# Performance work log

Measured on AMD Instinct MI355X. Metric: run time of the kernel, lower is better.

Reference implementation:

```python
import jax, jax.numpy as jnp
import numpy as np

N_NODES = 50000
N_EDGES = 500000
D = 128
C = 50


def setup_inputs() -> dict:
    key = jax.random.key(0)
    k1, k2, k3, k4, k5, k6 = jax.random.split(key, 6)
    h = jax.random.normal(k1, (N_NODES, D), dtype=jnp.float32)
    e = jax.random.normal(k2, (N_EDGES, D), dtype=jnp.float32)
    src = jax.random.randint(k3, (N_EDGES,), 0, N_NODES, dtype=jnp.int64)
    dst = jax.random.randint(k4, (N_EDGES,), 0, N_NODES, dtype=jnp.int64)
    # nn.Linear(3*D, C): weight [C, 3*D], bias [C]
    W = jax.random.normal(k5, (C, 3 * D), dtype=jnp.float32) * (1.0 / np.sqrt(3 * D))
    b = jax.random.normal(k6, (C,), dtype=jnp.float32) * 0.01
    return {"h": h, "e": e, "src": src, "dst": dst, "W": W, "b": b}


def reference(h, e, src, dst, W, b):
    # gather node feats for each edge endpoint, concat with edge feats
    h_u = h[src]                                   # [E, D]
    h_v = h[dst]                                   # [E, D]
    feats = jnp.concatenate([h_u, h_v, e], axis=1)  # [E, 3D]
    score = jnp.einsum('ef,cf->ec', feats, W) + b   # [E, C]
    return score
```

## Files before the change

kernel.cpp:

```cpp
#include <hip/hip_runtime.h>
#include <hip/hip_bf16.h>

#define N_EDGES_C 500000
#define D_C 128
#define C_C 50
#define K3_C 384
#define CPAD_C 64

typedef __attribute__((ext_vector_type(8))) short bf16x8;
typedef __attribute__((ext_vector_type(4))) float f32x4;

static __device__ inline short2 pack_bf16_2(float a, float b) {
    union { __hip_bfloat162 h; short2 s; } u;
    u.h = __float22bfloat162_rn(make_float2(a, b));
    return u.s;
}

__global__ void wconv_kernel(const float* __restrict__ W, short* __restrict__ WB) {
    int idx = blockIdx.x * blockDim.x + threadIdx.x;
    if (idx >= CPAD_C * K3_C) return;
    int c = idx / K3_C;
    int k = idx - c * K3_C;
    float v = (c < C_C) ? W[c * K3_C + k] : 0.0f;
    union { __hip_bfloat16 b; short s; } u;
    u.b = __float2bfloat16(v);
    WB[idx] = u.s;
}

__global__ __launch_bounds__(256) void edge_mlp_kernel(
    const float* __restrict__ h, const float* __restrict__ ef,
    const int* __restrict__ src, const int* __restrict__ dst,
    const short* __restrict__ WB, const float* __restrict__ bias,
    float* __restrict__ out)
{
    const int lane = threadIdx.x & 63;
    const int wave = threadIdx.x >> 6;
    const int m = lane & 15;
    const int q = lane >> 4;
    const int kq = q * 8;

    const long wave_base = (long)blockIdx.x * 256 + (long)wave * 64;

    const float* psrc[4];
    const float* pdst[4];
    const float* pef[4];
#pragma unroll
    for (int i = 0; i < 4; ++i) {
        long ei = wave_base + i * 16 + m;
        long eic = ei < N_EDGES_C ? ei : (long)(N_EDGES_C - 1);
        int si = src[eic];
        int di = dst[eic];
        psrc[i] = h + (long)si * D_C + kq;
        pdst[i] = h + (long)di * D_C + kq;
        pef[i]  = ef + eic * D_C + kq;
    }

    const short* wrow[4];
#pragma unroll
    for (int t = 0; t < 4; ++t)
        wrow[t] = WB + (t * 16 + m) * K3_C + kq;

    f32x4 acc[4][4];
#pragma unroll
    for (int i = 0; i < 4; ++i)
#pragma unroll
        for (int t = 0; t < 4; ++t)
            acc[i][t] = (f32x4){0.0f, 0.0f, 0.0f, 0.0f};

    auto kstep = [&](const float* const (&pr)[4], int koff, int ko) {
        bf16x8 bfr[4];
#pragma unroll
        for (int t = 0; t < 4; ++t)
            bfr[t] = *reinterpret_cast<const bf16x8*>(wrow[t] + ko);
#pragma unroll
        for (int i = 0; i < 4; ++i) {
            const float4 f0 = *reinterpret_cast<const float4*>(pr[i] + koff);
            const float4 f1 = *reinterpret_cast<const float4*>(pr[i] + koff + 4);
            short2 p0 = pack_bf16_2(f0.x, f0.y);
            short2 p1 = pack_bf16_2(f0.z, f0.w);
            short2 p2 = pack_bf16_2(f1.x, f1.y);
            short2 p3 = pack_bf16_2(f1.z, f1.w);
            bf16x8 afr = { p0.x, p0.y, p1.x, p1.y, p2.x, p2.y, p3.x, p3.y };
#pragma unroll
            for (int t = 0; t < 4; ++t)
                acc[i][t] = __builtin_amdgcn_mfma_f32_16x16x32_bf16(afr, bfr[t], acc[i][t], 0, 0, 0);
        }
    };

#pragma unroll
    for (int kk = 0; kk < 128; kk += 32) kstep(psrc, kk, kk);
#pragma unroll
    for (int kk = 0; kk < 128; kk += 32) kstep(pdst, kk, 128 + kk);
#pragma unroll
    for (int kk = 0; kk < 128; kk += 32) kstep(pef, kk, 256 + kk);

    float bv[4];
#pragma unroll
    for (int t = 0; t < 4; ++t) {
        int c = t * 16 + m;
        bv[t] = (c < C_C) ? bias[c] : 0.0f;
    }
#pragma unroll
    for (int i = 0; i < 4; ++i) {
        long er0 = wave_base + i * 16 + q * 4;
#pragma unroll
        for (int r = 0; r < 4; ++r) {
            long ei = er0 + r;
            if (ei < N_EDGES_C) {
#pragma unroll
                for (int t = 0; t < 4; ++t) {
                    int c = t * 16 + m;
                    if (c < C_C) out[ei * (long)C_C + c] = acc[i][t][r] + bv[t];
                }
            }
        }
    }
}

extern "C" void kernel_launch(void* const* d_in, const int* in_sizes, int n_in,
                              void* d_out, int out_size, void* d_ws, size_t ws_size,
                              hipStream_t stream) {
    const float* h  = (const float*)d_in[0];
    const float* ef = (const float*)d_in[1];
    const int*   src = (const int*)d_in[2];
    const int*   dst = (const int*)d_in[3];
    const float* W  = (const float*)d_in[4];
    const float* b  = (const float*)d_in[5];
    float* out = (float*)d_out;
    short* WB  = (short*)d_ws;

    wconv_kernel<<<(CPAD_C * K3_C + 255) / 256, 256, 0, stream>>>(W, WB);

    const int nblocks = (N_EDGES_C + 255) / 256;
    edge_mlp_kernel<<<nblocks, 256, 0, stream>>>(h, ef, src, dst, WB, b, out);
}
```

Before: 481.2 us.

## Precompute per-node projections then gather them per edge instead of gathering raw features

Splits the linear layer by linearity: h is projected once per node through the src and dst slices of W, with the bias folded in, into a node table HW of 50000x128 floats. The edge kernel then runs a GEMM over only the edge-feature slice and adds two gathered 50-float rows from HW. This removes the gather of two 128-float node rows per edge and two thirds of the edge-side MFMA work. In exchange it adds a node GEMM pass and about 25MB of workspace traffic, and it falls back to the old path when the workspace is too small.

```diff
diff --git a/kernel.cpp b/kernel.cpp
--- a/kernel.cpp
+++ b/kernel.cpp
@@ -1,6 +1,7 @@
 #include <hip/hip_runtime.h>
 #include <hip/hip_bf16.h>
 
+#define N_NODES_C 50000
 #define N_EDGES_C 500000
 #define D_C 128
 #define C_C 50
@@ -14,6 +15,146 @@
     union { __hip_bfloat162 h; short2 s; } u;
     u.h = __float22bfloat162_rn(make_float2(a, b));
     return u.s;
+}
+static __device__ inline short tobf(float v) {
+    union { __hip_bfloat16 b; short s; } u;
+    u.b = __float2bfloat16(v);
+    return u.s;
+}
+
+
+__global__ void wprep_kernel(const float* __restrict__ W,
+                             short* __restrict__ WB2, short* __restrict__ WB3) {
+    int idx = blockIdx.x * blockDim.x + threadIdx.x;
+    if (idx < 128 * 128) {
+        int r = idx >> 7, k = idx & 127;
+        float v = 0.0f;
+        if (r < C_C) v = W[r * K3_C + k];
+        else if (r >= 64 && r < 64 + C_C) v = W[(r - 64) * K3_C + 128 + k];
+        WB2[idx] = tobf(v);
+    } else if (idx < 128 * 128 + 64 * 128) {
+        int j = idx - 128 * 128;
+        int r = j >> 7, k = j & 127;
+        float v = (r < C_C) ? W[r * K3_C + 256 + k] : 0.0f;
+        WB3[j] = tobf(v);
+    }
+}
+
+__global__ __launch_bounds__(64) void node_gemm_kernel(
+    const float* __restrict__ h, const short* __restrict__ WB2,
+    const float* __restrict__ bias, float* __restrict__ HW)
+{
+    const int lane = threadIdx.x;
+    const int m = lane & 15, q = lane >> 4, kq = q * 8;
+    const long nbase = (long)blockIdx.x * 64;
+
+    bf16x8 A[4][4];
+#pragma unroll
+    for (int i = 0; i < 4; ++i) {
+        long ni = nbase + i * 16 + m;
+        if (ni >= N_NODES_C) ni = N_NODES_C - 1;
+        const float* pa = h + ni * D_C + kq;
+#pragma unroll
+        for (int kk = 0; kk < 4; ++kk) {
+            float4 f0 = *reinterpret_cast<const float4*>(pa + kk * 32);
+            float4 f1 = *reinterpret_cast<const float4*>(pa + kk * 32 + 4);
+            short2 p0 = pack_bf16_2(f0.x, f0.y), p1 = pack_bf16_2(f0.z, f0.w);
+            short2 p2 = pack_bf16_2(f1.x, f1.y), p3 = pack_bf16_2(f1.z, f1.w);
+            A[kk][i] = (bf16x8){p0.x, p0.y, p1.x, p1.y, p2.x, p2.y, p3.x, p3.y};
+        }
+    }
+#pragma unroll
+    for (int t = 0; t < 8; ++t) {
+        const short* wr = WB2 + (t * 16 + m) * D_C + kq;
+        f32x4 acc[4];
+#pragma unroll
+        for (int i = 0; i < 4; ++i) acc[i] = (f32x4){0.f, 0.f, 0.f, 0.f};
+#pragma unroll
+        for (int kk = 0; kk < 4; ++kk) {
+            bf16x8 bfr = *reinterpret_cast<const bf16x8*>(wr + kk * 32);
+#pragma unroll
+            for (int i = 0; i < 4; ++i)
+                acc[i] = __builtin_amdgcn_mfma_f32_16x16x32_bf16(A[kk][i], bfr, acc[i], 0, 0, 0);
+        }
+        int c = t * 16 + m;
+        float bv = (c < C_C) ? bias[c] : 0.0f;
+#pragma unroll
+        for (int i = 0; i < 4; ++i)
+#pragma unroll
+            for (int r = 0; r < 4; ++r) {
+                long ni = nbase + i * 16 + q * 4 + r;
+                if (ni < N_NODES_C) HW[ni * 128 + c] = acc[i][r] + bv;
+            }
+    }
+}
+
+__global__ __launch_bounds__(256) void edge_gemm_kernel(
+    const float* __restrict__ ef, const int* __restrict__ src,
+    const int* __restrict__ dst, const short* __restrict__ WB3,
+    const float* __restrict__ HW, float* __restrict__ out)
+{
+    const int lane = threadIdx.x & 63;
+    const int wave = threadIdx.x >> 6;
+    const int m = lane & 15, q = lane >> 4, kq = q * 8;
+    const long wave_base = (long)blockIdx.x * 256 + (long)wave * 64;
+
+    const float* pe[4];
+#pragma unroll
+    for (int i = 0; i < 4; ++i) {
+        long ei = wave_base + i * 16 + m;
+        if (ei >= N_EDGES_C) ei = N_EDGES_C - 1;
+        pe[i] = ef + ei * D_C + kq;
+    }
+    const short* wr[4];
+#pragma unroll
+    for (int t = 0; t < 4; ++t)
+        wr[t] = WB3 + (t * 16 + m) * D_C + kq;
+
+    f32x4 acc[4][4];
+#pragma unroll
+    for (int i = 0; i < 4; ++i)
+#pragma unroll
+        for (int t = 0; t < 4; ++t)
+            acc[i][t] = (f32x4){0.f, 0.f, 0.f, 0.f};
+
+#pragma unroll
+    for (int kk = 0; kk < 4; ++kk) {
+        bf16x8 bfr[4];
+#pragma unroll
+        for (int t = 0; t < 4; ++t)
+            bfr[t] = *reinterpret_cast<const bf16x8*>(wr[t] + kk * 32);
+#pragma unroll
+        for (int i = 0; i < 4; ++i) {
+            float4 f0 = *reinterpret_cast<const float4*>(pe[i] + kk * 32);
+            float4 f1 = *reinterpret_cast<const float4*>(pe[i] + kk * 32 + 4);
+            short2 p0 = pack_bf16_2(f0.x, f0.y), p1 = pack_bf16_2(f0.z, f0.w);
+            short2 p2 = pack_bf16_2(f1.x, f1.y), p3 = pack_bf16_2(f1.z, f1.w);
+            bf16x8 afr = {p0.x, p0.y, p1.x, p1.y, p2.x, p2.y, p3.x, p3.y};
+#pragma unroll
+            for (int t = 0; t < 4; ++t)
+                acc[i][t] = __builtin_amdgcn_mfma_f32_16x16x32_bf16(afr, bfr[t], acc[i][t], 0, 0, 0);
+        }
+    }
+
+#pragma unroll
+    for (int i = 0; i < 4; ++i) {
+#pragma unroll
+        for (int r = 0; r < 4; ++r) {
+            long ei = wave_base + i * 16 + q * 4 + r;
+            if (ei < N_EDGES_C) {
+                int si = src[ei];
+                int di = dst[ei];
+                const float* g1 = HW + (long)si * 128;
+                const float* g2 = HW + (long)di * 128 + 64;
+#pragma unroll
+                for (int t = 0; t < 4; ++t) {
+                    int c = t * 16 + m;
+                    if (c < C_C)
+                        out[ei * (long)C_C + c] = acc[i][t][r] + g1[c] + g2[c];
+                }
+            }
+        }
+    }
 }
 
 __global__ void wconv_kernel(const float* __restrict__ W, short* __restrict__ WB) {
@@ -22,9 +163,7 @@
     int c = idx / K3_C;
     int k = idx - c * K3_C;
     float v = (c < C_C) ? W[c * K3_C + k] : 0.0f;
-    union { __hip_bfloat16 b; short s; } u;
-    u.b = __float2bfloat16(v);
-    WB[idx] = u.s;
+    WB[idx] = tobf(v);
 }
 
 __global__ __launch_bounds__(256) void edge_mlp_kernel(
@@ -38,7 +177,6 @@
     const int m = lane & 15;
     const int q = lane >> 4;
     const int kq = q * 8;
-
     const long wave_base = (long)blockIdx.x * 256 + (long)wave * 64;
 
     const float* psrc[4];
@@ -54,7 +192,6 @@
         pdst[i] = h + (long)di * D_C + kq;
         pef[i]  = ef + eic * D_C + kq;
     }
-
     const short* wrow[4];
 #pragma unroll
     for (int t = 0; t < 4; ++t)
@@ -86,7 +223,6 @@
                 acc[i][t] = __builtin_amdgcn_mfma_f32_16x16x32_bf16(afr, bfr[t], acc[i][t], 0, 0, 0);
         }
     };
-
 #pragma unroll
     for (int kk = 0; kk < 128; kk += 32) kstep(psrc, kk, kk);
 #pragma unroll
@@ -120,17 +256,26 @@
 extern "C" void kernel_launch(void* const* d_in, const int* in_sizes, int n_in,
                               void* d_out, int out_size, void* d_ws, size_t ws_size,
                               hipStream_t stream) {
-    const float* h  = (const float*)d_in[0];
-    const float* ef = (const float*)d_in[1];
+    const float* h   = (const float*)d_in[0];
+    const float* ef  = (const float*)d_in[1];
     const int*   src = (const int*)d_in[2];
     const int*   dst = (const int*)d_in[3];
-    const float* W  = (const float*)d_in[4];
-    const float* b  = (const float*)d_in[5];
+    const float* W   = (const float*)d_in[4];
+    const float* b   = (const float*)d_in[5];
     float* out = (float*)d_out;
-    short* WB  = (short*)d_ws;
-
-    wconv_kernel<<<(CPAD_C * K3_C + 255) / 256, 256, 0, stream>>>(W, WB);
-
-    const int nblocks = (N_EDGES_C + 255) / 256;
-    edge_mlp_kernel<<<nblocks, 256, 0, stream>>>(h, ef, src, dst, WB, b, out);
-}
+
+    const size_t REQ = 49152 + (size_t)N_NODES_C * 128 * 4;
+    if (ws_size >= REQ) {
+        short* WB3 = (short*)d_ws;
+        short* WB2 = (short*)((char*)d_ws + 16384);
+        float* HW  = (float*)((char*)d_ws + 49152);
+
+        wprep_kernel<<<(128 * 128 + 64 * 128 + 255) / 256, 256, 0, stream>>>(W, WB2, WB3);
+        node_gemm_kernel<<<(N_NODES_C + 63) / 64, 64, 0, stream>>>(h, WB2, b, HW);
+        edge_gemm_kernel<<<(N_EDGES_C + 255) / 256, 256, 0, stream>>>(ef, src, dst, WB3, HW, out);
+    } else {
+        short* WB = (short*)d_ws;
+        wconv_kernel<<<(CPAD_C * K3_C + 255) / 256, 256, 0, stream>>>(W, WB);
+        edge_mlp_kernel<<<(N_EDGES_C + 255) / 256, 256, 0, stream>>>(h, ef, src, dst, WB, b, out);
+    }
+}
```

Result: faster. 458.0 us (-4.8%).
